# Kernel tuning notes

Measured on AMD Instinct MI355X. Metric: run time of the kernel, lower is better.

## Reference

```python
import jax, jax.numpy as jnp
import numpy as np

B, T_EN, T_DE, D_EN, D_DE, UNITS = 8, 512, 128, 512, 512, 256


def setup_inputs() -> dict:
    key = jax.random.key(0)
    k1, k2, k3, k4, k5, k6 = jax.random.split(key, 6)
    return {
        "en_seq": jax.random.normal(k1, (B, T_EN, D_EN), dtype=jnp.float32),
        "de_seq": jax.random.normal(k2, (B, T_DE, D_DE), dtype=jnp.float32),
        "mask_en": jax.random.randint(k3, (B, T_EN), 0, 2, dtype=jnp.int32),
        "w_en": jax.random.normal(k4, (D_EN, UNITS), dtype=jnp.float32) * (1.0 / np.sqrt(D_EN)),
        "w_de": jax.random.normal(k5, (D_DE, UNITS), dtype=jnp.float32) * (1.0 / np.sqrt(D_DE)),
        "nu": jax.random.normal(k6, (UNITS, 1), dtype=jnp.float32) * (1.0 / np.sqrt(UNITS)),
    }


def reference(en_seq, de_seq, mask_en, w_en, w_de, nu):
    # Additive (Bahdanau) attention scores.
    att_en = jnp.einsum('bed,du->beu', en_seq, w_en)   # [B, T_en, U]
    att_de = jnp.einsum('btd,du->btu', de_seq, w_de)   # [B, T_de, U]
    # co_m[b, j, i, u] = att_de[b, j, u] + att_en[b, i, u]
    co_m = jnp.tanh(att_de[:, :, None, :] + att_en[:, None, :, :])  # [B, T_de, T_en, U]
    mu = jnp.einsum('btiu,uo->bti', co_m, nu)          # [B, T_de, T_en]
    # mask: (m - 1) * 1e6 added to logits (m in {0,1})
    m = mask_en.astype(mu.dtype)                       # [B, T_en]
    mu = mu + ((m - 1.0) * 1000000.0)[:, None, :]
    return jax.nn.softmax(mu, axis=-1)                 # [B, T_de, T_en]
```

## Files before the change

### kernel.cpp

```cpp
#include <hip/hip_runtime.h>
#include <cstddef>
#include <cstdint>

#define B_    8
#define T_EN_ 512
#define T_DE_ 128
#define D_    512
#define U_    256

#define TANH_C 2.8853900817779268f
#define L2E_   1.4426950408889634f
#define TANH_CLAMP 0.99999994f

typedef float f32x4 __attribute__((ext_vector_type(4)));
typedef float f32x2 __attribute__((ext_vector_type(2)));
typedef short s16x8 __attribute__((ext_vector_type(8)));

__device__ __forceinline__ float fast_tanh_clamped(float x) {
  const float e = __builtin_amdgcn_exp2f(x * TANH_C);
  float t = fmaf(-2.0f, __builtin_amdgcn_rcpf(e + 1.0f), 1.0f);
  return fminf(fmaxf(t, -TANH_CLAMP), TANH_CLAMP);
}

__device__ __forceinline__ void split_bf16(float x, short& hi, short& lo) {
  const unsigned u = __float_as_uint(x);
  hi = (short)(u >> 16);
  const float hf = __uint_as_float(u & 0xffff0000u);
  const float lf = x - hf;
  lo = (short)(__float_as_uint(lf) >> 16);
}

__global__ __launch_bounds__(256) void prepack_kernel(
    const float* __restrict__ en, const float* __restrict__ de,
    const float* __restrict__ w_en, const float* __restrict__ w_de,
    short* __restrict__ en_hi, short* __restrict__ en_lo,
    short* __restrict__ de_hi, short* __restrict__ de_lo,
    short* __restrict__ wen_hi, short* __restrict__ wen_lo,
    short* __restrict__ wde_hi, short* __restrict__ wde_lo) {
  const int blk = blockIdx.x;
  const int tid = threadIdx.x;
  float v[8];
  short* ph;
  short* pl;
  size_t ub;

  if (blk < 1280) {
    const int gu = blk * 256 + tid;
    const int n = gu & 15;
    const int g = (gu >> 4) & 3;
    const int s = (gu >> 6) & 15;
    const int rb = gu >> 10;
    const float* src;
    if (rb < 256) {
      const int b = rb >> 5, t = rb & 31;
      src = en + ((size_t)rb * 16 + n) * D_;
      ub = ((size_t)((b * 16 + s) * 32 + t) * 4 + g) * 16 + n;
      ph = en_hi; pl = en_lo;
    } else {
      const int t64 = rb - 256;
      src = de + ((size_t)t64 * 16 + n) * D_;
      ub = ((size_t)(s * 64 + t64) * 4 + g) * 16 + n;
      ph = de_hi; pl = de_lo;
    }
    const int kb = s * 32 + g * 4;
    const float4 fa = *(const float4*)(src + kb);
    const float4 fb = *(const float4*)(src + kb + 16);
    v[0] = fa.x; v[1] = fa.y; v[2] = fa.z; v[3] = fa.w;
    v[4] = fb.x; v[5] = fb.y; v[6] = fb.z; v[7] = fb.w;
  } else {
    const int wb = blk - 1280;
    const bool is_en = wb < 64;
    const int wq = wb & 63;
    const int s = wq >> 2, USq = wq & 3;
    const int n = tid & 15;
    const int g = (tid >> 4) & 3;
    const int US = USq * 4 + (tid >> 6);
    const float* W = is_en ? w_en : w_de;
    ph = is_en ? wen_hi : wde_hi;
    pl = is_en ? wen_lo : wde_lo;
    #pragma unroll
    for (int e = 0; e < 8; ++e) {
      const int k = s * 32 + g * 4 + (e & 3) + 16 * (e >> 2);
      v[e] = W[(size_t)k * U_ + US * 16 + n];
    }
    ub = ((size_t)(s * 16 + US) * 4 + g) * 16 + n;
  }

  s16x8 h8, l8;
  #pragma unroll
  for (int e = 0; e < 8; ++e) {
    short h, l;
    split_bf16(v[e], h, l);
    h8[e] = h; l8[e] = l;
  }
  *(s16x8*)(ph + ub * 8) = h8;
  *(s16x8*)(pl + ub * 8) = l8;
}

__global__ __launch_bounds__(256) void mfma_proj_kernel(
    const short* __restrict__ en_hi, const short* __restrict__ en_lo,
    const short* __restrict__ de_hi, const short* __restrict__ de_lo,
    const short* __restrict__ wen_hi, const short* __restrict__ wen_lo,
    const short* __restrict__ wde_hi, const short* __restrict__ wde_lo,
    float* __restrict__ Et, float* __restrict__ de_t) {
  const int blk = blockIdx.x;
  const int tid = threadIdx.x;
  const int lane = tid & 63;
  const int wv = tid >> 6;
  const int rl = lane >> 4, cl = lane & 15;

  f32x4 acc[2] = {};
  s16x8 bufA[6], bufB[6];

  if (blk < 512) {
    const int b  = blk >> 6;
    const int uh = (blk >> 5) & 1;
    const int it = blk & 31;
    const int US0 = uh * 8 + wv * 2;

#define LOAD_EN(DST, S)                                                   \
    { const size_t oa0 = ((size_t)((S) * 16 + US0) * 64 + lane) * 8;      \
      const size_t ob  = ((size_t)((b * 16 + (S)) * 32 + it) * 64 + lane) * 8; \
      DST[0] = *(const s16x8*)(wen_hi + oa0);                             \
      DST[1] = *(const s16x8*)(wen_lo + oa0);                             \
      DST[2] = *(const s16x8*)(wen_hi + oa0 + 512);                       \
      DST[3] = *(const s16x8*)(wen_lo + oa0 + 512);                       \
      DST[4] = *(const s16x8*)(en_hi + ob);                               \
      DST[5] = *(const s16x8*)(en_lo + ob); }
#define MFMA_EN(S)                                                        \
    { acc[0] = __builtin_amdgcn_mfma_f32_16x16x32_bf16(S[0], S[4], acc[0], 0, 0, 0); \
      acc[0] = __builtin_amdgcn_mfma_f32_16x16x32_bf16(S[0], S[5], acc[0], 0, 0, 0); \
      acc[0] = __builtin_amdgcn_mfma_f32_16x16x32_bf16(S[1], S[4], acc[0], 0, 0, 0); \
      acc[1] = __builtin_amdgcn_mfma_f32_16x16x32_bf16(S[2], S[4], acc[1], 0, 0, 0); \
      acc[1] = __builtin_amdgcn_mfma_f32_16x16x32_bf16(S[2], S[5], acc[1], 0, 0, 0); \
      acc[1] = __builtin_amdgcn_mfma_f32_16x16x32_bf16(S[3], S[4], acc[1], 0, 0, 0); }

    LOAD_EN(bufA, 0)
    for (int s = 0; s < 16; s += 2) {
      LOAD_EN(bufB, s + 1)
      MFMA_EN(bufA)
      if (s + 2 < 16) LOAD_EN(bufA, s + 2)
      MFMA_EN(bufB)
    }
#undef LOAD_EN
#undef MFMA_EN

    #pragma unroll
    for (int us = 0; us < 2; ++us) {
      #pragma unroll
      for (int r = 0; r < 4; ++r) {
        const int u = (US0 + us) * 16 + rl * 4 + r;
        const int i = it * 16 + cl;
        Et[((size_t)b * U_ + u) * T_EN_ + i] = fast_tanh_clamped(acc[us][r]);
      }
    }
  } else {
    const int y = blk - 512;
    const int t64 = y >> 1;
    const int uh = y & 1;
    const int US0 = uh * 8 + wv * 2;

#define LOAD_DE(DST, S)                                                   \
    { const size_t oa = ((size_t)((S) * 64 + t64) * 64 + lane) * 8;       \
      const size_t ob = ((size_t)((S) * 16 + US0) * 64 + lane) * 8;       \
      DST[0] = *(const s16x8*)(de_hi + oa);                               \
      DST[1] = *(const s16x8*)(de_lo + oa);                               \
      DST[2] = *(const s16x8*)(wde_hi + ob);                              \
      DST[3] = *(const s16x8*)(wde_lo + ob);                              \
      DST[4] = *(const s16x8*)(wde_hi + ob + 512);                        \
      DST[5] = *(const s16x8*)(wde_lo + ob + 512); }
#define MFMA_DE(S)                                                        \
    { acc[0] = __builtin_amdgcn_mfma_f32_16x16x32_bf16(S[0], S[2], acc[0], 0, 0, 0); \
      acc[0] = __builtin_amdgcn_mfma_f32_16x16x32_bf16(S[0], S[3], acc[0], 0, 0, 0); \
      acc[0] = __builtin_amdgcn_mfma_f32_16x16x32_bf16(S[1], S[2], acc[0], 0, 0, 0); \
      acc[1] = __builtin_amdgcn_mfma_f32_16x16x32_bf16(S[0], S[4], acc[1], 0, 0, 0); \
      acc[1] = __builtin_amdgcn_mfma_f32_16x16x32_bf16(S[0], S[5], acc[1], 0, 0, 0); \
      acc[1] = __builtin_amdgcn_mfma_f32_16x16x32_bf16(S[1], S[4], acc[1], 0, 0, 0); }

    LOAD_DE(bufA, 0)
    for (int s = 0; s < 16; s += 2) {
      LOAD_DE(bufB, s + 1)
      MFMA_DE(bufA)
      if (s + 2 < 16) LOAD_DE(bufA, s + 2)
      MFMA_DE(bufB)
    }
#undef LOAD_DE
#undef MFMA_DE

    #pragma unroll
    for (int us = 0; us < 2; ++us) {
      #pragma unroll
      for (int r = 0; r < 4; ++r) {
        const int j = t64 * 16 + rl * 4 + r;
        const int u = (US0 + us) * 16 + cl;
        de_t[(size_t)j * U_ + u] = fast_tanh_clamped(acc[us][r]);
      }
    }
  }
}

__global__ __launch_bounds__(512) void attn_mu_softmax_kernel(
    const float* __restrict__ Et, const float* __restrict__ de_t,
    const float* __restrict__ nu, const int* __restrict__ mask,
    float* __restrict__ out) {
  __shared__ f32x4 Lp_s[4][U_ / 2];
  __shared__ f32x2 nv2_s[U_ / 2];
  __shared__ float mu_p[8][4][T_EN_];

  const int tid  = threadIdx.x;
  const int lane = tid & 63;
  const int w    = tid >> 6;
  const int b    = blockIdx.x & 7;
  const int jg   = blockIdx.x >> 3;
  const int j0   = jg * 4;

  {
    const int jl = tid >> 7;
    const int p  = tid & 127;
    const float2 Av = *(const float2*)(de_t + (size_t)(b * T_DE_ + j0 + jl) * U_ + 2 * p);
    const float2 nv = *(const float2*)(nu + 2 * p);
    f32x4 L;
    L[0] = Av.x; L[1] = Av.y; L[2] = nv.x * Av.x; L[3] = nv.y * Av.y;
    Lp_s[jl][p] = L;
    if (tid < 128) {
      const float2 n2 = *(const float2*)(nu + 2 * tid);
      f32x2 v; v[0] = n2.x; v[1] = n2.y;
      nv2_s[tid] = v;
    }
  }
  __syncthreads();

  const int pb = w * 16;
  const float* __restrict__ EbA =
      Et + ((size_t)b * U_ + 2 * pb) * T_EN_ + lane * 4;

  const f32x4 one4 = {1.f, 1.f, 1.f, 1.f};
  f32x4 accA[4] = {}, accB[4] = {};

  f32x4 E1Aa, E1Ba, E2Aa, E2Ba, E1Ab, E1Bb, E2Ab, E2Bb;
  f32x4 La[4], Lb[4];
  f32x2 nva, nvb;

#define LOADP(SUF, P)                                                     \
  { const float* e1 = EbA + (size_t)(2 * (P)) * T_EN_;                    \
    const float* e2 = e1 + T_EN_;                                         \
    E1A##SUF = *(const f32x4*)(e1);                                       \
    E1B##SUF = *(const f32x4*)(e1 + 256);                                 \
    E2A##SUF = *(const f32x4*)(e2);                                       \
    E2B##SUF = *(const f32x4*)(e2 + 256);                                 \
    L##SUF[0] = Lp_s[0][pb + (P)];                                        \
    L##SUF[1] = Lp_s[1][pb + (P)];                                        \
    L##SUF[2] = Lp_s[2][pb + (P)];                                        \
    L##SUF[3] = Lp_s[3][pb + (P)];                                        \
    nv##SUF = nv2_s[pb + (P)]; }

#define COMPP(SUF)                                                        \
  { const f32x4 T1A = E1A##SUF * nv##SUF[0];                              \
    const f32x4 T1B = E1B##SUF * nv##SUF[0];                              \
    const f32x4 T2A = E2A##SUF * nv##SUF[1];                              \
    const f32x4 T2B = E2B##SUF * nv##SUF[1];                              \
    _Pragma("unroll")                                                     \
    for (int jl = 0; jl < 4; ++jl) {                                      \
      const f32x4 Lc = L##SUF[jl];                                        \
      { const f32x4 d1 = E1A##SUF * Lc[0] + one4;                         \
        const f32x4 d2 = E2A##SUF * Lc[1] + one4;                         \
        const f32x4 n1 = T1A + Lc[2];                                     \
        const f32x4 n2 = T2A + Lc[3];                                     \
        const f32x4 Nn = n1 * d2 + n2 * d1;                               \
        const f32x4 Dd = d1 * d2;                                         \
        f32x4 r;                                                          \
        r[0] = __builtin_amdgcn_rcpf(Dd[0]);                              \
        r[1] = __builtin_amdgcn_rcpf(Dd[1]);                              \
        r[2] = __builtin_amdgcn_rcpf(Dd[2]);                              \
        r[3] = __builtin_amdgcn_rcpf(Dd[3]);                              \
        accA[jl] = Nn * r + accA[jl]; }                                   \
      { const f32x4 d1 = E1B##SUF * Lc[0] + one4;                         \
        const f32x4 d2 = E2B##SUF * Lc[1] + one4;                         \
        const f32x4 n1 = T1B + Lc[2];                                     \
        const f32x4 n2 = T2B + Lc[3];                                     \
        const f32x4 Nn = n1 * d2 + n2 * d1;                               \
        const f32x4 Dd = d1 * d2;                                         \
        f32x4 r;                                                          \
        r[0] = __builtin_amdgcn_rcpf(Dd[0]);                              \
        r[1] = __builtin_amdgcn_rcpf(Dd[1]);                              \
        r[2] = __builtin_amdgcn_rcpf(Dd[2]);                              \
        r[3] = __builtin_amdgcn_rcpf(Dd[3]);                              \
        accB[jl] = Nn * r + accB[jl]; }                                   \
    } }

  LOADP(a, 0)
  for (int p0 = 0; p0 < 16; p0 += 2) {
    LOADP(b, p0 + 1)
    COMPP(a)
    if (p0 + 2 < 16) LOADP(a, p0 + 2)
    COMPP(b)
  }
#undef LOADP
#undef COMPP

  #pragma unroll
  for (int jl = 0; jl < 4; ++jl) {
    *(f32x4*)&mu_p[w][jl][lane * 4] = accA[jl];
    *(f32x4*)&mu_p[w][jl][256 + lane * 4] = accB[jl];
  }
  __syncthreads();

  if (w < 4) {
    float vals[8];
    float mx = -3.0e38f;
    #pragma unroll
    for (int h = 0; h < 2; ++h) {
      f32x4 s = {0.f, 0.f, 0.f, 0.f};
      #pragma unroll
      for (int uo = 0; uo < 8; ++uo)
        s += *(const f32x4*)&mu_p[uo][w][h * 256 + lane * 4];
      const int4 mk = *(const int4*)(mask + b * T_EN_ + h * 256 + lane * 4);
      const float v0 = fmaf((float)mk.x - 1.f, 1.0e6f, s[0]);
      const float v1 = fmaf((float)mk.y - 1.f, 1.0e6f, s[1]);
      const float v2 = fmaf((float)mk.z - 1.f, 1.0e6f, s[2]);
      const float v3 = fmaf((float)mk.w - 1.f, 1.0e6f, s[3]);
      vals[h * 4 + 0] = v0; vals[h * 4 + 1] = v1;
      vals[h * 4 + 2] = v2; vals[h * 4 + 3] = v3;
      mx = fmaxf(mx, fmaxf(fmaxf(v0, v1), fmaxf(v2, v3)));
    }
    #pragma unroll
    for (int off = 32; off; off >>= 1) mx = fmaxf(mx, __shfl_xor(mx, off, 64));
    float sum = 0.0f;
    #pragma unroll
    for (int k = 0; k < 8; ++k) {
      const float e = __builtin_amdgcn_exp2f((vals[k] - mx) * L2E_);
      vals[k] = e;
      sum += e;
    }
    #pragma unroll
    for (int off = 32; off; off >>= 1) sum += __shfl_xor(sum, off, 64);
    const float inv = __builtin_amdgcn_rcpf(sum);
    float* op = out + (size_t)(b * T_DE_ + j0 + w) * T_EN_;
    #pragma unroll
    for (int h = 0; h < 2; ++h) {
      const float4 o = make_float4(vals[h * 4 + 0] * inv, vals[h * 4 + 1] * inv,
                                   vals[h * 4 + 2] * inv, vals[h * 4 + 3] * inv);
      *(float4*)(op + h * 256 + lane * 4) = o;
    }
  }
}

extern "C" void kernel_launch(void* const* d_in, const int* in_sizes, int n_in,
                              void* d_out, int out_size, void* d_ws, size_t ws_size,
                              hipStream_t stream) {
  const float* en   = (const float*)d_in[0];
  const float* de   = (const float*)d_in[1];
  const int*   mask = (const int*)d_in[2];
  const float* w_en = (const float*)d_in[3];
  const float* w_de = (const float*)d_in[4];
  const float* nu   = (const float*)d_in[5];
  float* out = (float*)d_out;

  float* Et   = (float*)d_ws;
  float* de_t = Et + (size_t)B_ * U_ * T_EN_;
  short* p    = (short*)(de_t + (size_t)B_ * T_DE_ * U_);
  short* en_hi = p;                 p += 2097152;
  short* en_lo = p;                 p += 2097152;
  short* de_hi = p;                 p += 524288;
  short* de_lo = p;                 p += 524288;
  short* wen_hi = p;                p += 131072;
  short* wen_lo = p;                p += 131072;
  short* wde_hi = p;                p += 131072;
  short* wde_lo = p;                p += 131072;

  prepack_kernel<<<dim3(1408), 256, 0, stream>>>(
      en, de, w_en, w_de, en_hi, en_lo, de_hi, de_lo,
      wen_hi, wen_lo, wde_hi, wde_lo);
  mfma_proj_kernel<<<dim3(640), 256, 0, stream>>>(
      en_hi, en_lo, de_hi, de_lo, wen_hi, wen_lo, wde_hi, wde_lo, Et, de_t);
  attn_mu_softmax_kernel<<<dim3(256), 512, 0, stream>>>(
      Et, de_t, nu, mask, out);
}
```

Before: 41.22 us.

## Fuse prepack, projection and softmax kernels into one persistent kernel with grid barriers

Replaces three kernel launches with a single persistent kernel of 256 blocks by 512 threads. Phases are separated by atomic-counter grid barriers, reset by a memset before each launch. The decoder projection is remapped to one 16x16 tile per wave instead of two, so the encoder and decoder GEMM work is spread across all waves. This is meant to remove the launch gaps and tail effects between kernels, at the cost of barrier spin time, lower occupancy during the prepack and GEMM phases, and a deadlock risk if not all 256 blocks are resident at once.

```diff
diff --git a/kernel.cpp b/kernel.cpp
--- a/kernel.cpp
+++ b/kernel.cpp
@@ -7,6 +7,9 @@
 #define T_DE_ 128
 #define D_    512
 #define U_    256
+
+#define NBLK  256
+#define NTHR  512
 
 #define TANH_C 2.8853900817779268f
 #define L2E_   1.4426950408889634f
@@ -30,317 +33,302 @@
   lo = (short)(__float_as_uint(lf) >> 16);
 }
 
-__global__ __launch_bounds__(256) void prepack_kernel(
+__device__ __forceinline__ void gridbar(int* cnt) {
+  __syncthreads();
+  if (threadIdx.x == 0) {
+    __hip_atomic_fetch_add(cnt, 1, __ATOMIC_ACQ_REL, __HIP_MEMORY_SCOPE_AGENT);
+    while (__hip_atomic_load(cnt, __ATOMIC_ACQUIRE, __HIP_MEMORY_SCOPE_AGENT) < NBLK) {
+      __builtin_amdgcn_s_sleep(8);
+    }
+  }
+  __syncthreads();
+}
+
+__global__ __launch_bounds__(512) void fused_attention_kernel(
     const float* __restrict__ en, const float* __restrict__ de,
     const float* __restrict__ w_en, const float* __restrict__ w_de,
+    const float* __restrict__ nu, const int* __restrict__ mask,
     short* __restrict__ en_hi, short* __restrict__ en_lo,
     short* __restrict__ de_hi, short* __restrict__ de_lo,
     short* __restrict__ wen_hi, short* __restrict__ wen_lo,
-    short* __restrict__ wde_hi, short* __restrict__ wde_lo) {
-  const int blk = blockIdx.x;
-  const int tid = threadIdx.x;
-  float v[8];
-  short* ph;
-  short* pl;
-  size_t ub;
-
-  if (blk < 1280) {
-    const int gu = blk * 256 + tid;
-    const int n = gu & 15;
-    const int g = (gu >> 4) & 3;
-    const int s = (gu >> 6) & 15;
-    const int rb = gu >> 10;
-    const float* src;
-    if (rb < 256) {
-      const int b = rb >> 5, t = rb & 31;
-      src = en + ((size_t)rb * 16 + n) * D_;
-      ub = ((size_t)((b * 16 + s) * 32 + t) * 4 + g) * 16 + n;
-      ph = en_hi; pl = en_lo;
-    } else {
-      const int t64 = rb - 256;
-      src = de + ((size_t)t64 * 16 + n) * D_;
-      ub = ((size_t)(s * 64 + t64) * 4 + g) * 16 + n;
-      ph = de_hi; pl = de_lo;
-    }
-    const int kb = s * 32 + g * 4;
-    const float4 fa = *(const float4*)(src + kb);
-    const float4 fb = *(const float4*)(src + kb + 16);
-    v[0] = fa.x; v[1] = fa.y; v[2] = fa.z; v[3] = fa.w;
-    v[4] = fb.x; v[5] = fb.y; v[6] = fb.z; v[7] = fb.w;
-  } else {
-    const int wb = blk - 1280;
-    const bool is_en = wb < 64;
-    const int wq = wb & 63;
-    const int s = wq >> 2, USq = wq & 3;
-    const int n = tid & 15;
-    const int g = (tid >> 4) & 3;
-    const int US = USq * 4 + (tid >> 6);
-    const float* W = is_en ? w_en : w_de;
-    ph = is_en ? wen_hi : wde_hi;
-    pl = is_en ? wen_lo : wde_lo;
-    #pragma unroll
-    for (int e = 0; e < 8; ++e) {
-      const int k = s * 32 + g * 4 + (e & 3) + 16 * (e >> 2);
-      v[e] = W[(size_t)k * U_ + US * 16 + n];
-    }
-    ub = ((size_t)(s * 16 + US) * 4 + g) * 16 + n;
-  }
-
-  s16x8 h8, l8;
-  #pragma unroll
-  for (int e = 0; e < 8; ++e) {
-    short h, l;
-    split_bf16(v[e], h, l);
-    h8[e] = h; l8[e] = l;
-  }
-  *(s16x8*)(ph + ub * 8) = h8;
-  *(s16x8*)(pl + ub * 8) = l8;
-}
-
-__global__ __launch_bounds__(256) void mfma_proj_kernel(
-    const short* __restrict__ en_hi, const short* __restrict__ en_lo,
-    const short* __restrict__ de_hi, const short* __restrict__ de_lo,
-    const short* __restrict__ wen_hi, const short* __restrict__ wen_lo,
-    const short* __restrict__ wde_hi, const short* __restrict__ wde_lo,
-    float* __restrict__ Et, float* __restrict__ de_t) {
-  const int blk = blockIdx.x;
-  const int tid = threadIdx.x;
-  const int lane = tid & 63;
-  const int wv = tid >> 6;
-  const int rl = lane >> 4, cl = lane & 15;
-
-  f32x4 acc[2] = {};
-  s16x8 bufA[6], bufB[6];
-
-  if (blk < 512) {
-    const int b  = blk >> 6;
-    const int uh = (blk >> 5) & 1;
-    const int it = blk & 31;
-    const int US0 = uh * 8 + wv * 2;
-
-#define LOAD_EN(DST, S)                                                   \
-    { const size_t oa0 = ((size_t)((S) * 16 + US0) * 64 + lane) * 8;      \
-      const size_t ob  = ((size_t)((b * 16 + (S)) * 32 + it) * 64 + lane) * 8; \
-      DST[0] = *(const s16x8*)(wen_hi + oa0);                             \
-      DST[1] = *(const s16x8*)(wen_lo + oa0);                             \
-      DST[2] = *(const s16x8*)(wen_hi + oa0 + 512);                       \
-      DST[3] = *(const s16x8*)(wen_lo + oa0 + 512);                       \
-      DST[4] = *(const s16x8*)(en_hi + ob);                               \
-      DST[5] = *(const s16x8*)(en_lo + ob); }
-#define MFMA_EN(S)                                                        \
-    { acc[0] = __builtin_amdgcn_mfma_f32_16x16x32_bf16(S[0], S[4], acc[0], 0, 0, 0); \
-      acc[0] = __builtin_amdgcn_mfma_f32_16x16x32_bf16(S[0], S[5], acc[0], 0, 0, 0); \
-      acc[0] = __builtin_amdgcn_mfma_f32_16x16x32_bf16(S[1], S[4], acc[0], 0, 0, 0); \
-      acc[1] = __builtin_amdgcn_mfma_f32_16x16x32_bf16(S[2], S[4], acc[1], 0, 0, 0); \
-      acc[1] = __builtin_amdgcn_mfma_f32_16x16x32_bf16(S[2], S[5], acc[1], 0, 0, 0); \
-      acc[1] = __builtin_amdgcn_mfma_f32_16x16x32_bf16(S[3], S[4], acc[1], 0, 0, 0); }
-
-    LOAD_EN(bufA, 0)
-    for (int s = 0; s < 16; s += 2) {
-      LOAD_EN(bufB, s + 1)
-      MFMA_EN(bufA)
-      if (s + 2 < 16) LOAD_EN(bufA, s + 2)
-      MFMA_EN(bufB)
-    }
-#undef LOAD_EN
-#undef MFMA_EN
-
-    #pragma unroll
-    for (int us = 0; us < 2; ++us) {
-      #pragma unroll
-      for (int r = 0; r < 4; ++r) {
-        const int u = (US0 + us) * 16 + rl * 4 + r;
-        const int i = it * 16 + cl;
-        Et[((size_t)b * U_ + u) * T_EN_ + i] = fast_tanh_clamped(acc[us][r]);
-      }
-    }
-  } else {
-    const int y = blk - 512;
-    const int t64 = y >> 1;
-    const int uh = y & 1;
-    const int US0 = uh * 8 + wv * 2;
-
-#define LOAD_DE(DST, S)                                                   \
-    { const size_t oa = ((size_t)((S) * 64 + t64) * 64 + lane) * 8;       \
-      const size_t ob = ((size_t)((S) * 16 + US0) * 64 + lane) * 8;       \
-      DST[0] = *(const s16x8*)(de_hi + oa);                               \
-      DST[1] = *(const s16x8*)(de_lo + oa);                               \
-      DST[2] = *(const s16x8*)(wde_hi + ob);                              \
-      DST[3] = *(const s16x8*)(wde_lo + ob);                              \
-      DST[4] = *(const s16x8*)(wde_hi + ob + 512);                        \
-      DST[5] = *(const s16x8*)(wde_lo + ob + 512); }
-#define MFMA_DE(S)                                                        \
-    { acc[0] = __builtin_amdgcn_mfma_f32_16x16x32_bf16(S[0], S[2], acc[0], 0, 0, 0); \
-      acc[0] = __builtin_amdgcn_mfma_f32_16x16x32_bf16(S[0], S[3], acc[0], 0, 0, 0); \
-      acc[0] = __builtin_amdgcn_mfma_f32_16x16x32_bf16(S[1], S[2], acc[0], 0, 0, 0); \
-      acc[1] = __builtin_amdgcn_mfma_f32_16x16x32_bf16(S[0], S[4], acc[1], 0, 0, 0); \
-      acc[1] = __builtin_amdgcn_mfma_f32_16x16x32_bf16(S[0], S[5], acc[1], 0, 0, 0); \
-      acc[1] = __builtin_amdgcn_mfma_f32_16x16x32_bf16(S[1], S[4], acc[1], 0, 0, 0); }
-
-    LOAD_DE(bufA, 0)
-    for (int s = 0; s < 16; s += 2) {
-      LOAD_DE(bufB, s + 1)
-      MFMA_DE(bufA)
-      if (s + 2 < 16) LOAD_DE(bufA, s + 2)
-      MFMA_DE(bufB)
-    }
-#undef LOAD_DE
-#undef MFMA_DE
-
-    #pragma unroll
-    for (int us = 0; us < 2; ++us) {
-      #pragma unroll
-      for (int r = 0; r < 4; ++r) {
-        const int j = t64 * 16 + rl * 4 + r;
-        const int u = (US0 + us) * 16 + cl;
-        de_t[(size_t)j * U_ + u] = fast_tanh_clamped(acc[us][r]);
-      }
-    }
-  }
-}
-
-__global__ __launch_bounds__(512) void attn_mu_softmax_kernel(
-    const float* __restrict__ Et, const float* __restrict__ de_t,
-    const float* __restrict__ nu, const int* __restrict__ mask,
-    float* __restrict__ out) {
+    short* __restrict__ wde_hi, short* __restrict__ wde_lo,
+    float* __restrict__ Et, float* __restrict__ de_t,
+    float* __restrict__ out, int* bar) {
   __shared__ f32x4 Lp_s[4][U_ / 2];
   __shared__ f32x2 nv2_s[U_ / 2];
   __shared__ float mu_p[8][4][T_EN_];
 
-  const int tid  = threadIdx.x;
-  const int lane = tid & 63;
-  const int w    = tid >> 6;
-  const int b    = blockIdx.x & 7;
-  const int jg   = blockIdx.x >> 3;
-  const int j0   = jg * 4;
+  const int lane = threadIdx.x & 63;
+  const int rl = lane >> 4, cl = lane & 15;
+
+  for (int gu = blockIdx.x * NTHR + threadIdx.x; gu < 1408 * 256; gu += NBLK * NTHR) {
+    const int blk = gu >> 8;
+    const int tid = gu & 255;
+    float v[8];
+    short *ph, *pl;
+    size_t ub;
+
+    if (blk < 1280) {
+      const int n = gu & 15;
+      const int g = (gu >> 4) & 3;
+      const int s = (gu >> 6) & 15;
+      const int rb = gu >> 10;
+      const float* src;
+      if (rb < 256) {
+        const int b = rb >> 5, t = rb & 31;
+        src = en + ((size_t)rb * 16 + n) * D_;
+        ub = ((size_t)((b * 16 + s) * 32 + t) * 4 + g) * 16 + n;
+        ph = en_hi; pl = en_lo;
+      } else {
+        const int t64 = rb - 256;
+        src = de + ((size_t)t64 * 16 + n) * D_;
+        ub = ((size_t)(s * 64 + t64) * 4 + g) * 16 + n;
+        ph = de_hi; pl = de_lo;
+      }
+      const int kb = s * 32 + g * 4;
+      const float4 fa = *(const float4*)(src + kb);
+      const float4 fb = *(const float4*)(src + kb + 16);
+      v[0] = fa.x; v[1] = fa.y; v[2] = fa.z; v[3] = fa.w;
+      v[4] = fb.x; v[5] = fb.y; v[6] = fb.z; v[7] = fb.w;
+    } else {
+      const int wb = blk - 1280;
+      const bool is_en = wb < 64;
+      const int wq = wb & 63;
+      const int s = wq >> 2, USq = wq & 3;
+      const int n = tid & 15;
+      const int g = (tid >> 4) & 3;
+      const int US = USq * 4 + (tid >> 6);
+      const float* W = is_en ? w_en : w_de;
+      ph = is_en ? wen_hi : wde_hi;
+      pl = is_en ? wen_lo : wde_lo;
+      #pragma unroll
+      for (int e = 0; e < 8; ++e) {
+        const int k = s * 32 + g * 4 + (e & 3) + 16 * (e >> 2);
+        v[e] = W[(size_t)k * U_ + US * 16 + n];
+      }
+      ub = ((size_t)(s * 16 + US) * 4 + g) * 16 + n;
+    }
+
+    s16x8 h8, l8;
+    #pragma unroll
+    for (int e = 0; e < 8; ++e) {
+      short h, l;
+      split_bf16(v[e], h, l);
+      h8[e] = h; l8[e] = l;
+    }
+    *(s16x8*)(ph + ub * 8) = h8;
+    *(s16x8*)(pl + ub * 8) = l8;
+  }
+
+  gridbar(bar);
 
   {
-    const int jl = tid >> 7;
-    const int p  = tid & 127;
-    const float2 Av = *(const float2*)(de_t + (size_t)(b * T_DE_ + j0 + jl) * U_ + 2 * p);
-    const float2 nv = *(const float2*)(nu + 2 * p);
-    f32x4 L;
-    L[0] = Av.x; L[1] = Av.y; L[2] = nv.x * Av.x; L[3] = nv.y * Av.y;
-    Lp_s[jl][p] = L;
-    if (tid < 128) {
-      const float2 n2 = *(const float2*)(nu + 2 * tid);
-      f32x2 v; v[0] = n2.x; v[1] = n2.y;
-      nv2_s[tid] = v;
+    const int gw = blockIdx.x * 8 + (threadIdx.x >> 6);
+    {
+      const int b = gw >> 8, uh = (gw >> 7) & 1, it = (gw >> 2) & 31, wv = gw & 3;
+      const int US0 = uh * 8 + wv * 2;
+      f32x4 acc[2] = {};
+      s16x8 bufA[6], bufB[6];
+
+#define LOAD_EN(DST, S)                                                   \
+      { const size_t oa0 = ((size_t)((S) * 16 + US0) * 64 + lane) * 8;    \
+        const size_t ob  = ((size_t)((b * 16 + (S)) * 32 + it) * 64 + lane) * 8; \
+        DST[0] = *(const s16x8*)(wen_hi + oa0);                           \
+        DST[1] = *(const s16x8*)(wen_lo + oa0);                           \
+        DST[2] = *(const s16x8*)(wen_hi + oa0 + 512);                     \
+        DST[3] = *(const s16x8*)(wen_lo + oa0 + 512);                     \
+        DST[4] = *(const s16x8*)(en_hi + ob);                             \
+        DST[5] = *(const s16x8*)(en_lo + ob); }
+#define MFMA_EN(S)                                                        \
+      { acc[0] = __builtin_amdgcn_mfma_f32_16x16x32_bf16(S[0], S[4], acc[0], 0, 0, 0); \
+        acc[0] = __builtin_amdgcn_mfma_f32_16x16x32_bf16(S[0], S[5], acc[0], 0, 0, 0); \
+        acc[0] = __builtin_amdgcn_mfma_f32_16x16x32_bf16(S[1], S[4], acc[0], 0, 0, 0); \
+        acc[1] = __builtin_amdgcn_mfma_f32_16x16x32_bf16(S[2], S[4], acc[1], 0, 0, 0); \
+        acc[1] = __builtin_amdgcn_mfma_f32_16x16x32_bf16(S[2], S[5], acc[1], 0, 0, 0); \
+        acc[1] = __builtin_amdgcn_mfma_f32_16x16x32_bf16(S[3], S[4], acc[1], 0, 0, 0); }
+
+      LOAD_EN(bufA, 0)
+      for (int s = 0; s < 16; s += 2) {
+        LOAD_EN(bufB, s + 1)
+        MFMA_EN(bufA)
+        if (s + 2 < 16) LOAD_EN(bufA, s + 2)
+        MFMA_EN(bufB)
+      }
+#undef LOAD_EN
+#undef MFMA_EN
+
+      #pragma unroll
+      for (int us = 0; us < 2; ++us) {
+        #pragma unroll
+        for (int r = 0; r < 4; ++r) {
+          const int u = (US0 + us) * 16 + rl * 4 + r;
+          const int i = it * 16 + cl;
+          Et[((size_t)b * U_ + u) * T_EN_ + i] = fast_tanh_clamped(acc[us][r]);
+        }
+      }
+    }
+    if (gw < 1024) {
+      const int t64 = gw >> 4;
+      const int US  = gw & 15;
+      f32x4 acc = {};
+      #pragma unroll 2
+      for (int s = 0; s < 16; ++s) {
+        const size_t oa = ((size_t)(s * 64 + t64) * 64 + lane) * 8;
+        const size_t ob = ((size_t)(s * 16 + US) * 64 + lane) * 8;
+        const s16x8 ah = *(const s16x8*)(de_hi + oa);
+        const s16x8 al = *(const s16x8*)(de_lo + oa);
+        const s16x8 wh = *(const s16x8*)(wde_hi + ob);
+        const s16x8 wl = *(const s16x8*)(wde_lo + ob);
+        acc = __builtin_amdgcn_mfma_f32_16x16x32_bf16(ah, wh, acc, 0, 0, 0);
+        acc = __builtin_amdgcn_mfma_f32_16x16x32_bf16(ah, wl, acc, 0, 0, 0);
+        acc = __builtin_amdgcn_mfma_f32_16x16x32_bf16(al, wh, acc, 0, 0, 0);
+      }
+      #pragma unroll
+      for (int r = 0; r < 4; ++r) {
+        const int j = t64 * 16 + rl * 4 + r;
+        const int u = US * 16 + cl;
+        de_t[(size_t)j * U_ + u] = fast_tanh_clamped(acc[r]);
+      }
     }
   }
-  __syncthreads();
-
-  const int pb = w * 16;
-  const float* __restrict__ EbA =
-      Et + ((size_t)b * U_ + 2 * pb) * T_EN_ + lane * 4;
-
-  const f32x4 one4 = {1.f, 1.f, 1.f, 1.f};
-  f32x4 accA[4] = {}, accB[4] = {};
-
-  f32x4 E1Aa, E1Ba, E2Aa, E2Ba, E1Ab, E1Bb, E2Ab, E2Bb;
-  f32x4 La[4], Lb[4];
-  f32x2 nva, nvb;
+
+  gridbar(bar + 1);
+
+  {
+    const int tid  = threadIdx.x;
+    const int kw   = tid >> 6;
+    const int b    = blockIdx.x & 7;
+    const int jg   = blockIdx.x >> 3;
+    const int j0   = jg * 4;
+
+    {
+      const int jl = tid >> 7;
+      const int p  = tid & 127;
+      const float2 Av = *(const float2*)(de_t + (size_t)(b * T_DE_ + j0 + jl) * U_ + 2 * p);
+      const float2 nv = *(const float2*)(nu + 2 * p);
+      f32x4 L;
+      L[0] = Av.x; L[1] = Av.y; L[2] = nv.x * Av.x; L[3] = nv.y * Av.y;
+      Lp_s[jl][p] = L;
+      if (tid < 128) {
+        const float2 n2 = *(const float2*)(nu + 2 * tid);
+        f32x2 v; v[0] = n2.x; v[1] = n2.y;
+        nv2_s[tid] = v;
+      }
+    }
+    __syncthreads();
+
+    const int pb = kw * 16;
+    const float* __restrict__ EbA =
+        Et + ((size_t)b * U_ + 2 * pb) * T_EN_ + lane * 4;
+
+    const f32x4 one4 = {1.f, 1.f, 1.f, 1.f};
+    f32x4 accA[4] = {}, accB[4] = {};
+
+    f32x4 E1Aa, E1Ba, E2Aa, E2Ba, E1Ab, E1Bb, E2Ab, E2Bb;
+    f32x4 La[4], Lb[4];
+    f32x2 nva, nvb;
 
 #define LOADP(SUF, P)                                                     \
-  { const float* e1 = EbA + (size_t)(2 * (P)) * T_EN_;                    \
-    const float* e2 = e1 + T_EN_;                                         \
-    E1A##SUF = *(const f32x4*)(e1);                                       \
-    E1B##SUF = *(const f32x4*)(e1 + 256);                                 \
-    E2A##SUF = *(const f32x4*)(e2);                                       \
-    E2B##SUF = *(const f32x4*)(e2 + 256);                                 \
-    L##SUF[0] = Lp_s[0][pb + (P)];                                        \
-    L##SUF[1] = Lp_s[1][pb + (P)];                                        \
-    L##SUF[2] = Lp_s[2][pb + (P)];                                        \
-    L##SUF[3] = Lp_s[3][pb + (P)];                                        \
-    nv##SUF = nv2_s[pb + (P)]; }
+    { const float* e1 = EbA + (size_t)(2 * (P)) * T_EN_;                  \
+      const float* e2 = e1 + T_EN_;                                       \
+      E1A##SUF = *(const f32x4*)(e1);                                     \
+      E1B##SUF = *(const f32x4*)(e1 + 256);                               \
+      E2A##SUF = *(const f32x4*)(e2);                                     \
+      E2B##SUF = *(const f32x4*)(e2 + 256);                               \
+      L##SUF[0] = Lp_s[0][pb + (P)];                                      \
+      L##SUF[1] = Lp_s[1][pb + (P)];                                      \
+      L##SUF[2] = Lp_s[2][pb + (P)];                                      \
+      L##SUF[3] = Lp_s[3][pb + (P)];                                      \
+      nv##SUF = nv2_s[pb + (P)]; }
 
 #define COMPP(SUF)                                                        \
-  { const f32x4 T1A = E1A##SUF * nv##SUF[0];                              \
-    const f32x4 T1B = E1B##SUF * nv##SUF[0];                              \
-    const f32x4 T2A = E2A##SUF * nv##SUF[1];                              \
-    const f32x4 T2B = E2B##SUF * nv##SUF[1];                              \
-    _Pragma("unroll")                                                     \
-    for (int jl = 0; jl < 4; ++jl) {                                      \
-      const f32x4 Lc = L##SUF[jl];                                        \
-      { const f32x4 d1 = E1A##SUF * Lc[0] + one4;                         \
-        const f32x4 d2 = E2A##SUF * Lc[1] + one4;                         \
-        const f32x4 n1 = T1A + Lc[2];                                     \
-        const f32x4 n2 = T2A + Lc[3];                                     \
-        const f32x4 Nn = n1 * d2 + n2 * d1;                               \
-        const f32x4 Dd = d1 * d2;                                         \
-        f32x4 r;                                                          \
-        r[0] = __builtin_amdgcn_rcpf(Dd[0]);                              \
-        r[1] = __builtin_amdgcn_rcpf(Dd[1]);                              \
-        r[2] = __builtin_amdgcn_rcpf(Dd[2]);                              \
-        r[3] = __builtin_amdgcn_rcpf(Dd[3]);                              \
-        accA[jl] = Nn * r + accA[jl]; }                                   \
-      { const f32x4 d1 = E1B##SUF * Lc[0] + one4;                         \
-        const f32x4 d2 = E2B##SUF * Lc[1] + one4;                         \
-        const f32x4 n1 = T1B + Lc[2];                                     \
-        const f32x4 n2 = T2B + Lc[3];                                     \
-        const f32x4 Nn = n1 * d2 + n2 * d1;                               \
-        const f32x4 Dd = d1 * d2;                                         \
-        f32x4 r;                                                          \
-        r[0] = __builtin_amdgcn_rcpf(Dd[0]);                              \
-        r[1] = __builtin_amdgcn_rcpf(Dd[1]);                              \
-        r[2] = __builtin_amdgcn_rcpf(Dd[2]);                              \
-        r[3] = __builtin_amdgcn_rcpf(Dd[3]);                              \
-        accB[jl] = Nn * r + accB[jl]; }                                   \
-    } }
-
-  LOADP(a, 0)
-  for (int p0 = 0; p0 < 16; p0 += 2) {
-    LOADP(b, p0 + 1)
-    COMPP(a)
-    if (p0 + 2 < 16) LOADP(a, p0 + 2)
-    COMPP(b)
-  }
+    { const f32x4 T1A = E1A##SUF * nv##SUF[0];                            \
+      const f32x4 T1B = E1B##SUF * nv##SUF[0];                            \
+      const f32x4 T2A = E2A##SUF * nv##SUF[1];                            \
+      const f32x4 T2B = E2B##SUF * nv##SUF[1];                            \
+      _Pragma("unroll")                                                   \
+      for (int jl = 0; jl < 4; ++jl) {                                    \
+        const f32x4 Lc = L##SUF[jl];                                      \
+        { const f32x4 d1 = E1A##SUF * Lc[0] + one4;                       \
+          const f32x4 d2 = E2A##SUF * Lc[1] + one4;                       \
+          const f32x4 n1 = T1A + Lc[2];                                   \
+          const f32x4 n2 = T2A + Lc[3];                                   \
+          const f32x4 Nn = n1 * d2 + n2 * d1;                             \
+          const f32x4 Dd = d1 * d2;                                       \
+          f32x4 r;                                                        \
+          r[0] = __builtin_amdgcn_rcpf(Dd[0]);                            \
+          r[1] = __builtin_amdgcn_rcpf(Dd[1]);                            \
+          r[2] = __builtin_amdgcn_rcpf(Dd[2]);                            \
+          r[3] = __builtin_amdgcn_rcpf(Dd[3]);                            \
+          accA[jl] = Nn * r + accA[jl]; }                                 \
+        { const f32x4 d1 = E1B##SUF * Lc[0] + one4;                       \
+          const f32x4 d2 = E2B##SUF * Lc[1] + one4;                       \
+          const f32x4 n1 = T1B + Lc[2];                                   \
+          const f32x4 n2 = T2B + Lc[3];                                   \
+          const f32x4 Nn = n1 * d2 + n2 * d1;                             \
+          const f32x4 Dd = d1 * d2;                                       \
+          f32x4 r;                                                        \
+          r[0] = __builtin_amdgcn_rcpf(Dd[0]);                            \
+          r[1] = __builtin_amdgcn_rcpf(Dd[1]);                            \
+          r[2] = __builtin_amdgcn_rcpf(Dd[2]);                            \
+          r[3] = __builtin_amdgcn_rcpf(Dd[3]);                            \
+          accB[jl] = Nn * r + accB[jl]; }                                 \
+      } }
+
+    LOADP(a, 0)
+    for (int p0 = 0; p0 < 16; p0 += 2) {
+      LOADP(b, p0 + 1)
+      COMPP(a)
+      if (p0 + 2 < 16) LOADP(a, p0 + 2)
+      COMPP(b)
+    }
 #undef LOADP
 #undef COMPP
 
-  #pragma unroll
-  for (int jl = 0; jl < 4; ++jl) {
-    *(f32x4*)&mu_p[w][jl][lane * 4] = accA[jl];
-    *(f32x4*)&mu_p[w][jl][256 + lane * 4] = accB[jl];
-  }
-  __syncthreads();
-
-  if (w < 4) {
-    float vals[8];
-    float mx = -3.0e38f;
     #pragma unroll
-    for (int h = 0; h < 2; ++h) {
-      f32x4 s = {0.f, 0.f, 0.f, 0.f};
-      #pragma unroll
-      for (int uo = 0; uo < 8; ++uo)
-        s += *(const f32x4*)&mu_p[uo][w][h * 256 + lane * 4];
-      const int4 mk = *(const int4*)(mask + b * T_EN_ + h * 256 + lane * 4);
-      const float v0 = fmaf((float)mk.x - 1.f, 1.0e6f, s[0]);
-      const float v1 = fmaf((float)mk.y - 1.f, 1.0e6f, s[1]);
-      const float v2 = fmaf((float)mk.z - 1.f, 1.0e6f, s[2]);
-      const float v3 = fmaf((float)mk.w - 1.f, 1.0e6f, s[3]);
-      vals[h * 4 + 0] = v0; vals[h * 4 + 1] = v1;
-      vals[h * 4 + 2] = v2; vals[h * 4 + 3] = v3;
-      mx = fmaxf(mx, fmaxf(fmaxf(v0, v1), fmaxf(v2, v3)));
-    }
-    #pragma unroll
-    for (int off = 32; off; off >>= 1) mx = fmaxf(mx, __shfl_xor(mx, off, 64));
-    float sum = 0.0f;
-    #pragma unroll
-    for (int k = 0; k < 8; ++k) {
-      const float e = __builtin_amdgcn_exp2f((vals[k] - mx) * L2E_);
-      vals[k] = e;
-      sum += e;
-    }
-    #pragma unroll
-    for (int off = 32; off; off >>= 1) sum += __shfl_xor(sum, off, 64);
-    const float inv = __builtin_amdgcn_rcpf(sum);
-    float* op = out + (size_t)(b * T_DE_ + j0 + w) * T_EN_;
-    #pragma unroll
-    for (int h = 0; h < 2; ++h) {
-      const float4 o = make_float4(vals[h * 4 + 0] * inv, vals[h * 4 + 1] * inv,
-                                   vals[h * 4 + 2] * inv, vals[h * 4 + 3] * inv);
-      *(float4*)(op + h * 256 + lane * 4) = o;
+    for (int jl = 0; jl < 4; ++jl) {
+      *(f32x4*)&mu_p[kw][jl][lane * 4] = accA[jl];
+      *(f32x4*)&mu_p[kw][jl][256 + lane * 4] = accB[jl];
+    }
+    __syncthreads();
+
+    if (kw < 4) {
+      float vals[8];
+      float mx = -3.0e38f;
+      #pragma unroll
+      for (int h = 0; h < 2; ++h) {
+        f32x4 s = {0.f, 0.f, 0.f, 0.f};
+        #pragma unroll
+        for (int uo = 0; uo < 8; ++uo)
+          s += *(const f32x4*)&mu_p[uo][kw][h * 256 + lane * 4];
+        const int4 mk = *(const int4*)(mask + b * T_EN_ + h * 256 + lane * 4);
+        const float v0 = fmaf((float)mk.x - 1.f, 1.0e6f, s[0]);
+        const float v1 = fmaf((float)mk.y - 1.f, 1.0e6f, s[1]);
+        const float v2 = fmaf((float)mk.z - 1.f, 1.0e6f, s[2]);
+        const float v3 = fmaf((float)mk.w - 1.f, 1.0e6f, s[3]);
+        vals[h * 4 + 0] = v0; vals[h * 4 + 1] = v1;
+        vals[h * 4 + 2] = v2; vals[h * 4 + 3] = v3;
+        mx = fmaxf(mx, fmaxf(fmaxf(v0, v1), fmaxf(v2, v3)));
+      }
+      #pragma unroll
+      for (int off = 32; off; off >>= 1) mx = fmaxf(mx, __shfl_xor(mx, off, 64));
+      float sum = 0.0f;
+      #pragma unroll
+      for (int k = 0; k < 8; ++k) {
+        const float e = __builtin_amdgcn_exp2f((vals[k] - mx) * L2E_);
+        vals[k] = e;
+        sum += e;
+      }
+      #pragma unroll
+      for (int off = 32; off; off >>= 1) sum += __shfl_xor(sum, off, 64);
+      const float inv = __builtin_amdgcn_rcpf(sum);
+      float* op = out + (size_t)(b * T_DE_ + j0 + kw) * T_EN_;
+      #pragma unroll
+      for (int h = 0; h < 2; ++h) {
+        const float4 o = make_float4(vals[h * 4 + 0] * inv, vals[h * 4 + 1] * inv,
+                                     vals[h * 4 + 2] * inv, vals[h * 4 + 3] * inv);
+        *(float4*)(op + h * 256 + lane * 4) = o;
+      }
     }
   }
 }
@@ -367,12 +355,11 @@
   short* wen_lo = p;                p += 131072;
   short* wde_hi = p;                p += 131072;
   short* wde_lo = p;                p += 131072;
-
-  prepack_kernel<<<dim3(1408), 256, 0, stream>>>(
-      en, de, w_en, w_de, en_hi, en_lo, de_hi, de_lo,
-      wen_hi, wen_lo, wde_hi, wde_lo);
-  mfma_proj_kernel<<<dim3(640), 256, 0, stream>>>(
-      en_hi, en_lo, de_hi, de_lo, wen_hi, wen_lo, wde_hi, wde_lo, Et, de_t);
-  attn_mu_softmax_kernel<<<dim3(256), 512, 0, stream>>>(
-      Et, de_t, nu, mask, out);
-}
+  int* bar = (int*)p;
+
+  hipMemsetAsync(bar, 0, 2 * sizeof(int), stream);
+  fused_attention_kernel<<<dim3(NBLK), dim3(NTHR), 0, stream>>>(
+      en, de, w_en, w_de, nu, mask,
+      en_hi, en_lo, de_hi, de_lo, wen_hi, wen_lo, wde_hi, wde_lo,
+      Et, de_t, out, bar);
+}
```

Measured after the change: 110.2 us. 167% more time.
